# Kernel optimization log

Measured on AMD Instinct MI355X. Metric: run time of the kernel, lower is better.

## Reference

```python
import jax, jax.numpy as jnp
import numpy as np

B, T, C = 1, 4096, 1024
H = 16
D = C // H  # 64
LN_EPS = 1e-5


def layer_norm(x, g, b):
    mu = jnp.mean(x, axis=-1, keepdims=True)
    var = jnp.mean(jnp.square(x - mu), axis=-1, keepdims=True)
    return (x - mu) * jax.lax.rsqrt(var + LN_EPS) * g + b


def setup_inputs() -> dict:
    key = jax.random.key(0)
    ks = jax.random.split(key, 8)
    s = 0.02
    return {
        "x": jax.random.normal(ks[0], (B, T, C), dtype=jnp.float32),
        "ln1_g": jnp.ones((C,), jnp.float32),
        "ln1_b": jnp.zeros((C,), jnp.float32),
        "Wqkv": jax.random.normal(ks[1], (C, 3 * C), dtype=jnp.float32) * s,
        "bqkv": jnp.zeros((3 * C,), jnp.float32),
        "Wo": jax.random.normal(ks[2], (C, C), dtype=jnp.float32) * s,
        "bo": jnp.zeros((C,), jnp.float32),
        "ln2_g": jnp.ones((C,), jnp.float32),
        "ln2_b": jnp.zeros((C,), jnp.float32),
        "W1": jax.random.normal(ks[3], (C, 4 * C), dtype=jnp.float32) * s,
        "b1": jnp.zeros((4 * C,), jnp.float32),
        "W2": jax.random.normal(ks[4], (4 * C, C), dtype=jnp.float32) * s,
        "b2": jnp.zeros((C,), jnp.float32),
    }


def reference(x, ln1_g, ln1_b, Wqkv, bqkv, Wo, bo, ln2_g, ln2_b, W1, b1, W2, b2):
    b, t, c = x.shape
    x_norm = layer_norm(x, ln1_g, ln1_b)
    qkv = x_norm @ Wqkv + bqkv                      # [B,T,3C]
    qkv = qkv.reshape(b, t, 3, H, D).transpose(2, 0, 3, 1, 4)  # [3,B,H,T,D]
    Q, K, V = qkv[0], qkv[1], qkv[2]
    scores = jnp.einsum("bhtd,bhsd->bhts", Q, K) / jnp.sqrt(jnp.float32(D))
    causal = jnp.tril(jnp.ones((t, t), dtype=bool))  # [T,T]
    scores = jnp.where(causal[None, None], scores, -jnp.inf)
    weights = jax.nn.softmax(scores, axis=-1)
    attn = jnp.einsum("bhts,bhsd->bhtd", weights, V)  # [B,H,T,D]
    attn = attn.transpose(0, 2, 1, 3).reshape(b, t, c)
    x = x + (attn @ Wo + bo)
    h = layer_norm(x, ln2_g, ln2_b)
    h = jax.nn.gelu(h @ W1 + b1, approximate=False) @ W2 + b2
    return x + h
```

## Files before the change

### kernel.cpp

```cpp
#include <hip/hip_runtime.h>
#include <math.h>

typedef __bf16 bf16_t;
typedef __attribute__((ext_vector_type(8))) __bf16 bf16x8;
typedef __attribute__((ext_vector_type(4))) __bf16 bf16x4;
typedef __attribute__((ext_vector_type(4))) float f32x4;
typedef __attribute__((ext_vector_type(16))) float f32x16;
typedef __attribute__((ext_vector_type(4))) unsigned int u32x4;

#define T_LEN 4096
#define C_DIM 1024
#define NH 16
#define HD 64

__device__ __forceinline__ void gload_lds16(const void* g, void* l) {
    __builtin_amdgcn_global_load_lds(
        (__attribute__((address_space(1))) void*)(g),
        (__attribute__((address_space(3))) void*)(l), 16, 0, 0);
}

__device__ __forceinline__ f32x4 mfma16(bf16x8 a, bf16x8 b, f32x4 c) {
    return __builtin_amdgcn_mfma_f32_16x16x32_bf16(a, b, c, 0, 0, 0);
}

__device__ __forceinline__ f32x16 mfma32(bf16x8 a, bf16x8 b, f32x16 c) {
    return __builtin_amdgcn_mfma_f32_32x32x16_bf16(a, b, c, 0, 0, 0);
}

__device__ __forceinline__ float gelu_exact(float v) {
    return 0.5f * v * (1.0f + erff(v * 0.7071067811865476f));
}

__device__ __forceinline__ void make_frags2(const f32x16 s, bf16x8& fx, bf16x8& fy) {
    unsigned a0, a1, b0, b1;
    asm("v_cvt_pk_bf16_f32 %0, %1, %2" : "=v"(a0) : "v"(s[0]), "v"(s[1]));
    asm("v_cvt_pk_bf16_f32 %0, %1, %2" : "=v"(a1) : "v"(s[2]), "v"(s[3]));
    asm("v_cvt_pk_bf16_f32 %0, %1, %2" : "=v"(b0) : "v"(s[4]), "v"(s[5]));
    asm("v_cvt_pk_bf16_f32 %0, %1, %2" : "=v"(b1) : "v"(s[6]), "v"(s[7]));
    asm("v_permlane32_swap_b32 %0, %1" : "+v"(a0), "+v"(b0));
    asm("v_permlane32_swap_b32 %0, %1" : "+v"(a1), "+v"(b1));
    u32x4 wa = {a0, a1, b0, b1};
    fx = __builtin_bit_cast(bf16x8, wa);
    unsigned c0, c1, d0, d1;
    asm("v_cvt_pk_bf16_f32 %0, %1, %2" : "=v"(c0) : "v"(s[8]), "v"(s[9]));
    asm("v_cvt_pk_bf16_f32 %0, %1, %2" : "=v"(c1) : "v"(s[10]), "v"(s[11]));
    asm("v_cvt_pk_bf16_f32 %0, %1, %2" : "=v"(d0) : "v"(s[12]), "v"(s[13]));
    asm("v_cvt_pk_bf16_f32 %0, %1, %2" : "=v"(d1) : "v"(s[14]), "v"(s[15]));
    asm("v_permlane32_swap_b32 %0, %1" : "+v"(c0), "+v"(d0));
    asm("v_permlane32_swap_b32 %0, %1" : "+v"(c1), "+v"(d1));
    u32x4 wb = {c0, c1, d0, d1};
    fy = __builtin_bit_cast(bf16x8, wb);
}

__global__ __launch_bounds__(256) void transpose_all(
    const float* __restrict__ wqkv, const float* __restrict__ wo,
    const float* __restrict__ w1, const float* __restrict__ w2,
    bf16_t* __restrict__ oqkv, bf16_t* __restrict__ owo,
    bf16_t* __restrict__ ow1, bf16_t* __restrict__ ow2)
{
    __shared__ float tile[32][33];
    int s = blockIdx.x;
    const float* in; bf16_t* out; int R, C, NBX;
    if (s < 3072)      {            in = wqkv; out = oqkv; R = 1024; C = 3072; NBX = 96; }
    else if (s < 4096) { s -= 3072; in = wo;   out = owo;  R = 1024; C = 1024; NBX = 32; }
    else if (s < 8192) { s -= 4096; in = w1;   out = ow1;  R = 1024; C = 4096; NBX = 128; }
    else               { s -= 8192; in = w2;   out = ow2;  R = 4096; C = 1024; NBX = 32; }
    const int tx = threadIdx.x, ty = threadIdx.y;
    const int c0 = (s % NBX) * 32, r0 = (s / NBX) * 32;
#pragma unroll
    for (int j = 0; j < 4; ++j)
        tile[ty + j * 8][tx] = in[(size_t)(r0 + ty + j * 8) * C + c0 + tx];
    __syncthreads();
#pragma unroll
    for (int j = 0; j < 4; ++j)
        out[(size_t)(c0 + ty + j * 8) * R + r0 + tx] = (bf16_t)tile[tx][ty + j * 8];
}

__global__ __launch_bounds__(256) void vtrans(
    const bf16_t* __restrict__ qkv, bf16_t* __restrict__ vt)
{
    __shared__ bf16_t tile[32][33];
    const int tx = threadIdx.x, ty = threadIdx.y;
    const int h = blockIdx.z;
    const int t0 = blockIdx.x * 32, d0 = blockIdx.y * 32;
#pragma unroll
    for (int j = 0; j < 4; ++j)
        tile[ty + j * 8][tx] =
            qkv[(size_t)(t0 + ty + j * 8) * 3072 + 2048 + h * 64 + d0 + tx];
    __syncthreads();
#pragma unroll
    for (int j = 0; j < 4; ++j)
        vt[(size_t)h * (64 * 4096) + (size_t)(d0 + ty + j * 8) * 4096 + t0 + tx] =
            tile[tx][ty + j * 8];
}

__global__ __launch_bounds__(256) void ln_bf16(
    const float* __restrict__ x, const float* __restrict__ gam,
    const float* __restrict__ bet, bf16_t* __restrict__ out)
{
    const int row = blockIdx.x, t = threadIdx.x;
    const float4 v = *(const float4*)(x + (size_t)row * 1024 + t * 4);
    float s1 = v.x + v.y + v.z + v.w;
    float s2 = v.x * v.x + v.y * v.y + v.z * v.z + v.w * v.w;
#pragma unroll
    for (int m = 1; m < 64; m <<= 1) {
        s1 += __shfl_xor(s1, m);
        s2 += __shfl_xor(s2, m);
    }
    __shared__ float red[8];
    if ((t & 63) == 0) { red[(t >> 6) * 2] = s1; red[(t >> 6) * 2 + 1] = s2; }
    __syncthreads();
    s1 = red[0] + red[2] + red[4] + red[6];
    s2 = red[1] + red[3] + red[5] + red[7];
    const float mu = s1 * (1.0f / 1024.0f);
    const float inv = rsqrtf(s2 * (1.0f / 1024.0f) - mu * mu + 1e-5f);
    const float4 gg = *(const float4*)(gam + t * 4);
    const float4 bb = *(const float4*)(bet + t * 4);
    bf16x4 o;
    o[0] = (bf16_t)((v.x - mu) * inv * gg.x + bb.x);
    o[1] = (bf16_t)((v.y - mu) * inv * gg.y + bb.y);
    o[2] = (bf16_t)((v.z - mu) * inv * gg.z + bb.z);
    o[3] = (bf16_t)((v.w - mu) * inv * gg.w + bb.w);
    *(bf16x4*)(out + (size_t)row * 1024 + t * 4) = o;
}

template <int EPI>
__global__ __launch_bounds__(256, 2) void gemm_bt(
    const bf16_t* __restrict__ A, const bf16_t* __restrict__ Bt,
    const float* __restrict__ bias, const float* __restrict__ res,
    bf16_t* __restrict__ outb, float* __restrict__ outf,
    int M, int N, int Klen, int Kstr)
{
    __shared__ alignas(1024) bf16_t Alds[4][128 * 32];
    __shared__ alignas(1024) bf16_t Blds[4][128 * 32];
    const int t = threadIdx.x;
    const int lane = t & 63, w = t >> 6;
    const int wr = w >> 1, wc = w & 1;
    const int g = lane >> 4, ci = lane & 15;

    int bx, by, chunk = 0;
    if constexpr (EPI == 3) {
        const int flat = blockIdx.x + 8 * blockIdx.y;
        const int xcd = flat & 7, s = flat >> 3;
        chunk = s >> 5;
        const int s2 = s & 31;
        by = xcd * 4 + (s2 >> 3);
        bx = s2 & 7;
        A  += (size_t)chunk * Klen;
        Bt += (size_t)chunk * Klen;
    } else {
        const int NB = gridDim.x, MB = gridDim.y;
        const int flat = blockIdx.x + NB * blockIdx.y;
        const int xcd = flat & 7, slot = flat >> 3;
        by = xcd * (MB >> 3) + slot / NB;
        bx = slot % NB;
    }
    const int m0 = by * 128, n0 = bx * 128;

    f32x4 acc[4][4];
#pragma unroll
    for (int i = 0; i < 4; ++i)
#pragma unroll
        for (int j = 0; j < 4; ++j)
#pragma unroll
            for (int k = 0; k < 4; ++k) acc[i][j][k] = 0.0f;

    const int r0 = t >> 2;
    const int cc = (t & 3) * 8;
    const int nkt = Klen >> 5;

    auto stage = [&](int kt) {
        const int b = kt & 3;
        const int kk = kt * 32;
        char* aB = (char*)&Alds[b][0] + w * 1024;
        char* bB = (char*)&Blds[b][0] + w * 1024;
        gload_lds16(A + (size_t)(m0 + r0) * Kstr + kk + cc, aB);
        gload_lds16(A + (size_t)(m0 + r0 + 64) * Kstr + kk + cc, aB + 4096);
        gload_lds16(Bt + (size_t)(n0 + r0) * Kstr + kk + cc, bB);
        gload_lds16(Bt + (size_t)(n0 + r0 + 64) * Kstr + kk + cc, bB + 4096);
    };

    stage(0);
    if (nkt > 1) stage(1);
    for (int kt = 0; kt < nkt; ++kt) {
        if (kt + 2 < nkt) {
            stage(kt + 2);
            asm volatile("s_waitcnt vmcnt(8)" ::: "memory");
        } else if (kt + 1 < nkt) {
            asm volatile("s_waitcnt vmcnt(4)" ::: "memory");
        } else {
            asm volatile("s_waitcnt vmcnt(0)" ::: "memory");
        }
        __builtin_amdgcn_s_barrier();
        __builtin_amdgcn_sched_barrier(0);
        const int b = kt & 3;
        const bf16_t* ap = &Alds[b][0] + (wr * 64 + ci) * 32 + g * 8;
        const bf16_t* bp = &Blds[b][0] + (wc * 64 + ci) * 32 + g * 8;
        bf16x8 af[4], bf[4];
#pragma unroll
        for (int mt = 0; mt < 4; ++mt) af[mt] = *(const bf16x8*)(ap + mt * 16 * 32);
#pragma unroll
        for (int nt = 0; nt < 4; ++nt) bf[nt] = *(const bf16x8*)(bp + nt * 16 * 32);
        __builtin_amdgcn_s_setprio(1);
#pragma unroll
        for (int mt = 0; mt < 4; ++mt)
#pragma unroll
            for (int nt = 0; nt < 4; ++nt)
                acc[mt][nt] = mfma16(af[mt], bf[nt], acc[mt][nt]);
        __builtin_amdgcn_s_setprio(0);
    }

#pragma unroll
    for (int nt = 0; nt < 4; ++nt) {
        const int col = n0 + wc * 64 + nt * 16 + ci;
        const float bv = (EPI == 3) ? 0.0f : bias[col];
#pragma unroll
        for (int mt = 0; mt < 4; ++mt) {
            const int row = m0 + wr * 64 + mt * 16 + g * 4;
#pragma unroll
            for (int r = 0; r < 4; ++r) {
                float v = acc[mt][nt][r] + bv;
                if constexpr (EPI == 1) v = gelu_exact(v);
                if constexpr (EPI == 2) {
                    outf[(size_t)(row + r) * N + col] =
                        v + res[(size_t)(row + r) * N + col];
                } else if constexpr (EPI == 3) {
                    outf[((size_t)chunk * M + row + r) * N + col] = v;
                } else {
                    outb[(size_t)(row + r) * N + col] = (bf16_t)v;
                }
            }
        }
    }
}

__global__ __launch_bounds__(256) void w2_combine(
    const float* __restrict__ part, const float* __restrict__ bias,
    const float* __restrict__ res, float* __restrict__ out)
{
    const int row = blockIdx.x, t = threadIdx.x;
    const int c = t * 4;
    const float4 a = *(const float4*)(part + (size_t)row * 1024 + c);
    const float4 b = *(const float4*)(part + ((size_t)T_LEN + row) * 1024 + c);
    const float4 rr = *(const float4*)(res + (size_t)row * 1024 + c);
    const float4 bb = *(const float4*)(bias + c);
    float4 o;
    o.x = a.x + b.x + rr.x + bb.x;
    o.y = a.y + b.y + rr.y + bb.y;
    o.z = a.z + b.z + rr.z + bb.z;
    o.w = a.w + b.w + rr.w + bb.w;
    *(float4*)(out + (size_t)row * 1024 + c) = o;
}

template <int EPI>
__global__ __launch_bounds__(512, 2) void gemm256(
    const bf16_t* __restrict__ A, const bf16_t* __restrict__ Bt,
    const float* __restrict__ bias, bf16_t* __restrict__ outb,
    int M, int N, int K)
{
    __shared__ alignas(1024) bf16_t lds[2][2][256 * 64];
    const int t = threadIdx.x, lane = t & 63, w = t >> 6;
    const int g = lane >> 4, ci = lane & 15;
    const int wr = w >> 2, wc = w & 3;
    const int NB = gridDim.x;
    const int nwg = NB * gridDim.y;
    const int flat = blockIdx.x + NB * blockIdx.y;
    const int rix = (flat & 7) * (nwg >> 3) + (flat >> 3);
    const int m0 = (rix / NB) * 256, n0 = (rix % NB) * 256;
    const int NKT = K >> 6;

    f32x4 acc[8][4];
#pragma unroll
    for (int i = 0; i < 8; ++i)
#pragma unroll
        for (int j = 0; j < 4; ++j)
#pragma unroll
            for (int k2 = 0; k2 < 4; ++k2) acc[i][j][k2] = 0.0f;

    const int sw0 = (g ^ (ci & 7)) * 8;
    const int sw1 = ((4 + g) ^ (ci & 7)) * 8;

    auto stage = [&](int h, int ktile, int b) {
#pragma unroll
        for (int i = 0; i < 2; ++i) {
            const int idx = i * 512 + t;
            const int r = idx >> 3;
            const int c = (t & 7) ^ (r & 7);
            const bf16_t* src = ((h < 2) ? A : Bt)
                + (size_t)(((h < 2) ? m0 : n0) + (h & 1) * 128 + r) * K
                + ktile * 64 + c * 8;
            bf16_t* dst = &lds[b][h >> 1][(h & 1) * 8192] + (i * 512 + w * 64) * 8;
            gload_lds16(src, dst);
        }
    };

    bf16x8 a[4][2], b2[2][2][2];

    stage(0, 0, 0); stage(3, 0, 0); stage(1, 0, 0); stage(2, 0, 0);
    if (NKT > 1) { stage(0, 1, 1); stage(3, 1, 1); stage(1, 1, 1); }
    asm volatile("s_waitcnt vmcnt(6)" ::: "memory");
    __builtin_amdgcn_s_barrier();

    for (int kt = 0; kt < NKT; ++kt) {
        const int cur = kt & 1;
        const bf16_t* Ab = &lds[cur][0][0];
        const bf16_t* Bb = &lds[cur][1][0];

#pragma unroll
        for (int mi = 0; mi < 4; ++mi) {
            const bf16_t* ap = Ab + (wr * 64 + mi * 16 + ci) * 64;
            a[mi][0] = *(const bf16x8*)(ap + sw0);
            a[mi][1] = *(const bf16x8*)(ap + sw1);
        }
#pragma unroll
        for (int ni = 0; ni < 2; ++ni) {
            const bf16_t* bp = Bb + (wc * 32 + ni * 16 + ci) * 64;
            b2[0][ni][0] = *(const bf16x8*)(bp + sw0);
            b2[0][ni][1] = *(const bf16x8*)(bp + sw1);
        }
        if (kt + 1 < NKT) stage(2, kt + 1, cur ^ 1);
        __builtin_amdgcn_s_barrier();
        asm volatile("s_waitcnt lgkmcnt(0)" ::: "memory");
        __builtin_amdgcn_sched_barrier(0);
        __builtin_amdgcn_s_setprio(1);
#pragma unroll
        for (int mi = 0; mi < 4; ++mi)
#pragma unroll
            for (int ni = 0; ni < 2; ++ni) {
                acc[mi][ni] = mfma16(a[mi][0], b2[0][ni][0], acc[mi][ni]);
                acc[mi][ni] = mfma16(a[mi][1], b2[0][ni][1], acc[mi][ni]);
            }
        __builtin_amdgcn_s_setprio(0);
        __builtin_amdgcn_s_barrier();

#pragma unroll
        for (int ni = 0; ni < 2; ++ni) {
            const bf16_t* bp = Bb + (128 + wc * 32 + ni * 16 + ci) * 64;
            b2[1][ni][0] = *(const bf16x8*)(bp + sw0);
            b2[1][ni][1] = *(const bf16x8*)(bp + sw1);
        }
        if (kt + 2 < NKT) stage(0, kt + 2, cur);
        __builtin_amdgcn_s_barrier();
        asm volatile("s_waitcnt lgkmcnt(0)" ::: "memory");
        __builtin_amdgcn_sched_barrier(0);
        __builtin_amdgcn_s_setprio(1);
#pragma unroll
        for (int mi = 0; mi < 4; ++mi)
#pragma unroll
            for (int ni = 0; ni < 2; ++ni) {
                acc[mi][2 + ni] = mfma16(a[mi][0], b2[1][ni][0], acc[mi][2 + ni]);
                acc[mi][2 + ni] = mfma16(a[mi][1], b2[1][ni][1], acc[mi][2 + ni]);
            }
        __builtin_amdgcn_s_setprio(0);
        __builtin_amdgcn_s_barrier();

#pragma unroll
        for (int mi = 0; mi < 4; ++mi) {
            const bf16_t* ap = Ab + (128 + wr * 64 + mi * 16 + ci) * 64;
            a[mi][0] = *(const bf16x8*)(ap + sw0);
            a[mi][1] = *(const bf16x8*)(ap + sw1);
        }
        if (kt + 2 < NKT) stage(3, kt + 2, cur);
        __builtin_amdgcn_s_barrier();
        asm volatile("s_waitcnt lgkmcnt(0)" ::: "memory");
        __builtin_amdgcn_sched_barrier(0);
        __builtin_amdgcn_s_setprio(1);
#pragma unroll
        for (int mi = 0; mi < 4; ++mi)
#pragma unroll
            for (int ni = 0; ni < 2; ++ni) {
                acc[4 + mi][2 + ni] = mfma16(a[mi][0], b2[1][ni][0], acc[4 + mi][2 + ni]);
                acc[4 + mi][2 + ni] = mfma16(a[mi][1], b2[1][ni][1], acc[4 + mi][2 + ni]);
            }
        __builtin_amdgcn_s_setprio(0);
        __builtin_amdgcn_s_barrier();

        if (kt + 2 < NKT) stage(1, kt + 2, cur);
        __builtin_amdgcn_s_barrier();
        __builtin_amdgcn_s_setprio(1);
#pragma unroll
        for (int mi = 0; mi < 4; ++mi)
#pragma unroll
            for (int ni = 0; ni < 2; ++ni) {
                acc[4 + mi][ni] = mfma16(a[mi][0], b2[0][ni][0], acc[4 + mi][ni]);
                acc[4 + mi][ni] = mfma16(a[mi][1], b2[0][ni][1], acc[4 + mi][ni]);
            }
        __builtin_amdgcn_s_setprio(0);
        if (kt + 2 < NKT) asm volatile("s_waitcnt vmcnt(6)" ::: "memory");
        else              asm volatile("s_waitcnt vmcnt(0)" ::: "memory");
        __builtin_amdgcn_s_barrier();
    }

#pragma unroll
    for (int mrep = 0; mrep < 8; ++mrep) {
        const int row = m0 + (mrep >> 2) * 128 + wr * 64 + (mrep & 3) * 16 + g * 4;
#pragma unroll
        for (int nrep = 0; nrep < 4; ++nrep) {
            const int col = n0 + (nrep >> 1) * 128 + wc * 32 + (nrep & 1) * 16 + ci;
            const float bv = bias[col];
#pragma unroll
            for (int jr = 0; jr < 4; ++jr) {
                float v = acc[mrep][nrep][jr] + bv;
                if constexpr (EPI == 1) v = gelu_exact(v);
                outb[(size_t)(row + jr) * N + col] = (bf16_t)v;
            }
        }
    }
}

__global__ __launch_bounds__(256, 2) void attn_fwd(
    const bf16_t* __restrict__ qkv, const bf16_t* __restrict__ vt,
    bf16_t* __restrict__ opart, float* __restrict__ mlbuf)
{
    __shared__ alignas(1024) bf16_t Klds[2][64 * 64];
    __shared__ alignas(1024) bf16_t Vlds[2][64 * 64];
    const int t = threadIdx.x, lane = t & 63, w = t >> 6;
    const int hi = lane >> 5, li = lane & 31;
    const int lq = li >> 2;
    const int h = blockIdx.x;
    const int y = blockIdx.y;
    const int jj = y >> 4, v = y & 15;
    const int chunk = jj >> 1;
    const int qt = (jj == 0) ? v : (jj == 1) ? (31 - v) : (jj == 2) ? (16 + v) : (15 - v);
    const int q0 = qt * 128;
    const int qrow = q0 + w * 32 + li;
    const int wDiag = 2 * qt + (w >> 1);
    const int ktA = chunk ? (qt + 1) : 0;
    const int ktB = chunk ? (2 * qt + 2) : (qt + 1);
    const float C1 = 0.125f * 1.4426950408889634f;
    const float FM = 16.0f;

    bf16x8 qf[4];
#pragma unroll
    for (int ks = 0; ks < 4; ++ks)
        qf[ks] = *(const bf16x8*)(qkv + (size_t)qrow * 3072 + h * 64 + ks * 16 + hi * 8);
    bf16x8 ones8;
#pragma unroll
    for (int j = 0; j < 8; ++j) ones8[j] = (bf16_t)1.0f;

    f32x16 oacc[2], lacc;
#pragma unroll
    for (int r = 0; r < 16; ++r) { oacc[0][r] = 0.0f; oacc[1][r] = 0.0f; lacc[r] = 0.0f; }

    const int sr = t >> 3;
    const int sx = ((t & 7) ^ ((sr >> 2) & 7)) * 8;

    auto stageKV = [&](int kt, int b) {
        const size_t kbase = (size_t)(kt * 64) * 3072 + 1024 + h * 64 + sx;
        const size_t vbase = (size_t)h * 262144 + (size_t)kt * 64 + sx;
#pragma unroll
        for (int i = 0; i < 2; ++i) {
            gload_lds16(qkv + kbase + (size_t)(i * 32 + sr) * 3072,
                        (char*)&Klds[b][0] + (size_t)(i * 2048 + t * 8) * 2);
            gload_lds16(vt + vbase + (size_t)(i * 32 + sr) * 4096,
                        (char*)&Vlds[b][0] + (size_t)(i * 2048 + t * 8) * 2);
        }
    };

    stageKV(ktA, 0);
    for (int kt = ktA; kt < ktB; ++kt) {
        const int cur = (kt - ktA) & 1;
        asm volatile("s_waitcnt vmcnt(0)" ::: "memory");
        __syncthreads();
        if (kt + 1 < ktB) stageKV(kt + 1, cur ^ 1);

        if (kt <= wDiag) {
            const bf16_t* Kb = &Klds[cur][0];
            const bf16_t* Vb = &Vlds[cur][0];
            f32x16 s0, s1;
#pragma unroll
            for (int r = 0; r < 16; ++r) { s0[r] = 0.0f; s1[r] = 0.0f; }

            __builtin_amdgcn_s_setprio(1);
#pragma unroll
            for (int ks = 0; ks < 4; ++ks) {
                const int cs = ((ks * 2 + hi) ^ lq) * 8;
                s0 = mfma32(*(const bf16x8*)(Kb + li * 64 + cs), qf[ks], s0);
                s1 = mfma32(*(const bf16x8*)(Kb + (32 + li) * 64 + cs), qf[ks], s1);
            }
            __builtin_amdgcn_s_setprio(0);

            bf16x8 vf[4][2];
#pragma unroll
            for (int ks = 0; ks < 4; ++ks) {
                const int cs = ((ks * 2 + hi) ^ lq) * 8;
                vf[ks][0] = *(const bf16x8*)(Vb + li * 64 + cs);
                vf[ks][1] = *(const bf16x8*)(Vb + (32 + li) * 64 + cs);
            }

            if (kt == wDiag) {
                const int kb0 = kt * 64 + 4 * hi;
#pragma unroll
                for (int r = 0; r < 16; ++r) {
                    const int kp0 = kb0 + (r & 3) + 8 * (r >> 2);
                    if (kp0 > qrow) s0[r] = -1e30f;
                    if (kp0 + 32 > qrow) s1[r] = -1e30f;
                }
            }
#pragma unroll
            for (int r = 0; r < 16; ++r) {
                s0[r] = exp2f(fmaf(s0[r], C1, -FM));
                s1[r] = exp2f(fmaf(s1[r], C1, -FM));
            }

            bf16x8 pf[4];
            make_frags2(s0, pf[0], pf[1]);
            make_frags2(s1, pf[2], pf[3]);

            __builtin_amdgcn_s_setprio(1);
#pragma unroll
            for (int ks = 0; ks < 4; ++ks) {
                oacc[0] = mfma32(vf[ks][0], pf[ks], oacc[0]);
                oacc[1] = mfma32(vf[ks][1], pf[ks], oacc[1]);
                lacc    = mfma32(ones8,     pf[ks], lacc);
            }
            __builtin_amdgcn_s_setprio(0);
        }
        __syncthreads();
    }

    bf16_t* op = opart + ((size_t)chunk * T_LEN + qrow) * 1024 + h * 64 + hi * 4;
#pragma unroll
    for (int dblk = 0; dblk < 2; ++dblk)
#pragma unroll
        for (int gi = 0; gi < 4; ++gi) {
            bf16x4 o4;
#pragma unroll
            for (int j = 0; j < 4; ++j) o4[j] = (bf16_t)oacc[dblk][gi * 4 + j];
            *(bf16x4*)(op + dblk * 32 + gi * 8) = o4;
        }
    if (hi == 0) {
        float2 ml = make_float2(FM, lacc[0]);
        *(float2*)(mlbuf + (((size_t)chunk * T_LEN + qrow) * NH + h) * 2) = ml;
    }
}

__global__ __launch_bounds__(256) void attn_combine(
    const bf16_t* __restrict__ opart, const float* __restrict__ mlbuf,
    bf16_t* __restrict__ out)
{
    const int row = blockIdx.x, t = threadIdx.x;
    const int c = t * 4, h = c >> 6;
    const float2 ml0 = *(const float2*)(mlbuf + ((size_t)row * NH + h) * 2);
    const float2 ml1 = *(const float2*)(mlbuf + (((size_t)T_LEN + row) * NH + h) * 2);
    const float M = fmaxf(ml0.x, ml1.x);
    const float w0 = exp2f(ml0.x - M), w1 = exp2f(ml1.x - M);
    const float inv = 1.0f / (ml0.y * w0 + ml1.y * w1);
    const bf16x4 o0 = *(const bf16x4*)(opart + (size_t)row * 1024 + c);
    const bf16x4 o1 = *(const bf16x4*)(opart + ((size_t)T_LEN + row) * 1024 + c);
    bf16x4 o;
#pragma unroll
    for (int j = 0; j < 4; ++j)
        o[j] = (bf16_t)(((float)o0[j] * w0 + (float)o1[j] * w1) * inv);
    *(bf16x4*)(out + (size_t)row * 1024 + c) = o;
}

extern "C" void kernel_launch(void* const* d_in, const int* in_sizes, int n_in,
                              void* d_out, int out_size, void* d_ws, size_t ws_size,
                              hipStream_t stream)
{
    const float* x    = (const float*)d_in[0];
    const float* ln1g = (const float*)d_in[1];
    const float* ln1b = (const float*)d_in[2];
    const float* Wqkv = (const float*)d_in[3];
    const float* bqkv = (const float*)d_in[4];
    const float* Wo   = (const float*)d_in[5];
    const float* bo   = (const float*)d_in[6];
    const float* ln2g = (const float*)d_in[7];
    const float* ln2b = (const float*)d_in[8];
    const float* W1   = (const float*)d_in[9];
    const float* b1   = (const float*)d_in[10];
    const float* W2   = (const float*)d_in[11];
    const float* b2   = (const float*)d_in[12];
    float* outp = (float*)d_out;

    char* p = (char*)d_ws;
    bf16_t* WqkvT = (bf16_t*)p; p += (size_t)3072 * 1024 * 2;
    bf16_t* WoT   = (bf16_t*)p; p += (size_t)1024 * 1024 * 2;
    bf16_t* W1T   = (bf16_t*)p; p += (size_t)4096 * 1024 * 2;
    bf16_t* W2T   = (bf16_t*)p; p += (size_t)1024 * 4096 * 2;
    bf16_t* xn    = (bf16_t*)p; p += (size_t)4096 * 1024 * 2;
    bf16_t* qkv   = (bf16_t*)p; p += (size_t)4096 * 3072 * 2;
    bf16_t* vtb   = (bf16_t*)p; p += (size_t)16 * 64 * 4096 * 2;
    bf16_t* attnb = (bf16_t*)p; p += (size_t)4096 * 1024 * 2;
    float*  x2    = (float*)p;  p += (size_t)4096 * 1024 * 4;
    bf16_t* hb    = (bf16_t*)p; p += (size_t)4096 * 1024 * 2;
    bf16_t* g1    = (bf16_t*)p; p += (size_t)4096 * 4096 * 2;
    bf16_t* opart = (bf16_t*)p; p += (size_t)2 * 4096 * 1024 * 2;
    float*  mlbuf = (float*)p;  p += (size_t)2 * 4096 * 16 * 2 * 4;
    float*  w2part = (float*)p; p += (size_t)2 * 4096 * 1024 * 4;

    transpose_all<<<12288, dim3(32, 8), 0, stream>>>(Wqkv, Wo, W1, W2,
                                                     WqkvT, WoT, W1T, W2T);

    ln_bf16<<<4096, 256, 0, stream>>>(x, ln1g, ln1b, xn);
    gemm256<0><<<dim3(12, 16), 512, 0, stream>>>(xn, WqkvT, bqkv,
                                                 qkv, 4096, 3072, 1024);
    vtrans<<<dim3(128, 2, 16), dim3(32, 8), 0, stream>>>(qkv, vtb);
    attn_fwd<<<dim3(16, 64), 256, 0, stream>>>(qkv, vtb, opart, mlbuf);
    attn_combine<<<4096, 256, 0, stream>>>(opart, mlbuf, attnb);
    gemm_bt<2><<<dim3(8, 32), 256, 0, stream>>>(attnb, WoT, bo, x,
                                                nullptr, x2, 4096, 1024, 1024, 1024);
    ln_bf16<<<4096, 256, 0, stream>>>(x2, ln2g, ln2b, hb);
    gemm256<1><<<dim3(16, 16), 512, 0, stream>>>(hb, W1T, b1,
                                                 g1, 4096, 4096, 1024);
    gemm_bt<3><<<dim3(8, 64), 256, 0, stream>>>(g1, W2T, nullptr, nullptr,
                                                nullptr, w2part, 4096, 1024, 2048, 4096);
    w2_combine<<<4096, 256, 0, stream>>>(w2part, b2, x2, outp);
}
```

Measured before the change: 271.5 us.

## Fuse V transpose into QKV GEMM epilogue and simplify attention split combine

The QKV GEMM epilogue now writes the V columns straight into the per-head transposed layout, so the separate vtrans kernel and its extra read/write of V go away. Attention drops the stored running max because it uses a fixed max constant (FM), so the combine just adds the two partial outputs and the two row sums. The attention grid now visits query tiles from the heaviest first, with the two chunks interleaved, instead of the old balanced permutation. Risks: the V stores in the epilogue are scattered 8-byte writes, and the fixed-max softmax relies on scores staying within range.

Result: faster. 256.9 us (-5.4%).

```diff
diff --git a/kernel.cpp b/kernel.cpp
--- a/kernel.cpp
+++ b/kernel.cpp
@@ -76,24 +76,6 @@
         out[(size_t)(c0 + ty + j * 8) * R + r0 + tx] = (bf16_t)tile[tx][ty + j * 8];
 }
 
-__global__ __launch_bounds__(256) void vtrans(
-    const bf16_t* __restrict__ qkv, bf16_t* __restrict__ vt)
-{
-    __shared__ bf16_t tile[32][33];
-    const int tx = threadIdx.x, ty = threadIdx.y;
-    const int h = blockIdx.z;
-    const int t0 = blockIdx.x * 32, d0 = blockIdx.y * 32;
-#pragma unroll
-    for (int j = 0; j < 4; ++j)
-        tile[ty + j * 8][tx] =
-            qkv[(size_t)(t0 + ty + j * 8) * 3072 + 2048 + h * 64 + d0 + tx];
-    __syncthreads();
-#pragma unroll
-    for (int j = 0; j < 4; ++j)
-        vt[(size_t)h * (64 * 4096) + (size_t)(d0 + ty + j * 8) * 4096 + t0 + tx] =
-            tile[tx][ty + j * 8];
-}
-
 __global__ __launch_bounds__(256) void ln_bf16(
     const float* __restrict__ x, const float* __restrict__ gam,
     const float* __restrict__ bet, bf16_t* __restrict__ out)
@@ -256,7 +238,7 @@
 __global__ __launch_bounds__(512, 2) void gemm256(
     const bf16_t* __restrict__ A, const bf16_t* __restrict__ Bt,
     const float* __restrict__ bias, bf16_t* __restrict__ outb,
-    int M, int N, int K)
+    bf16_t* __restrict__ vtout, int M, int N, int K)
 {
     __shared__ alignas(1024) bf16_t lds[2][2][256 * 64];
     const int t = threadIdx.x, lane = t & 63, w = t >> 6;
@@ -398,11 +380,21 @@
         for (int nrep = 0; nrep < 4; ++nrep) {
             const int col = n0 + (nrep >> 1) * 128 + wc * 32 + (nrep & 1) * 16 + ci;
             const float bv = bias[col];
-#pragma unroll
-            for (int jr = 0; jr < 4; ++jr) {
-                float v = acc[mrep][nrep][jr] + bv;
-                if constexpr (EPI == 1) v = gelu_exact(v);
-                outb[(size_t)(row + jr) * N + col] = (bf16_t)v;
+            if (EPI == 2 && col >= 2048) {
+                const int cv = col - 2048;
+                bf16x4 o4;
+#pragma unroll
+                for (int jr = 0; jr < 4; ++jr)
+                    o4[jr] = (bf16_t)(acc[mrep][nrep][jr] + bv);
+                *(bf16x4*)(vtout + (size_t)(cv >> 6) * 262144
+                           + (size_t)(cv & 63) * 4096 + row) = o4;
+            } else {
+#pragma unroll
+                for (int jr = 0; jr < 4; ++jr) {
+                    float v = acc[mrep][nrep][jr] + bv;
+                    if constexpr (EPI == 1) v = gelu_exact(v);
+                    outb[(size_t)(row + jr) * N + col] = (bf16_t)v;
+                }
             }
         }
     }
@@ -410,7 +402,7 @@
 
 __global__ __launch_bounds__(256, 2) void attn_fwd(
     const bf16_t* __restrict__ qkv, const bf16_t* __restrict__ vt,
-    bf16_t* __restrict__ opart, float* __restrict__ mlbuf)
+    bf16_t* __restrict__ opart, float* __restrict__ lbuf)
 {
     __shared__ alignas(1024) bf16_t Klds[2][64 * 64];
     __shared__ alignas(1024) bf16_t Vlds[2][64 * 64];
@@ -419,9 +411,8 @@
     const int lq = li >> 2;
     const int h = blockIdx.x;
     const int y = blockIdx.y;
-    const int jj = y >> 4, v = y & 15;
-    const int chunk = jj >> 1;
-    const int qt = (jj == 0) ? v : (jj == 1) ? (31 - v) : (jj == 2) ? (16 + v) : (15 - v);
+    const int qt = 31 - (y >> 1);
+    const int chunk = y & 1;
     const int q0 = qt * 128;
     const int qrow = q0 + w * 32 + li;
     const int wDiag = 2 * qt + (w >> 1);
@@ -529,29 +520,25 @@
             for (int j = 0; j < 4; ++j) o4[j] = (bf16_t)oacc[dblk][gi * 4 + j];
             *(bf16x4*)(op + dblk * 32 + gi * 8) = o4;
         }
-    if (hi == 0) {
-        float2 ml = make_float2(FM, lacc[0]);
-        *(float2*)(mlbuf + (((size_t)chunk * T_LEN + qrow) * NH + h) * 2) = ml;
-    }
+    if (hi == 0)
+        lbuf[((size_t)chunk * T_LEN + qrow) * NH + h] = lacc[0];
 }
 
 __global__ __launch_bounds__(256) void attn_combine(
-    const bf16_t* __restrict__ opart, const float* __restrict__ mlbuf,
+    const bf16_t* __restrict__ opart, const float* __restrict__ lbuf,
     bf16_t* __restrict__ out)
 {
     const int row = blockIdx.x, t = threadIdx.x;
     const int c = t * 4, h = c >> 6;
-    const float2 ml0 = *(const float2*)(mlbuf + ((size_t)row * NH + h) * 2);
-    const float2 ml1 = *(const float2*)(mlbuf + (((size_t)T_LEN + row) * NH + h) * 2);
-    const float M = fmaxf(ml0.x, ml1.x);
-    const float w0 = exp2f(ml0.x - M), w1 = exp2f(ml1.x - M);
-    const float inv = 1.0f / (ml0.y * w0 + ml1.y * w1);
+    const float l0 = lbuf[(size_t)row * NH + h];
+    const float l1 = lbuf[((size_t)T_LEN + row) * NH + h];
+    const float inv = 1.0f / (l0 + l1);
     const bf16x4 o0 = *(const bf16x4*)(opart + (size_t)row * 1024 + c);
     const bf16x4 o1 = *(const bf16x4*)(opart + ((size_t)T_LEN + row) * 1024 + c);
     bf16x4 o;
 #pragma unroll
     for (int j = 0; j < 4; ++j)
-        o[j] = (bf16_t)(((float)o0[j] * w0 + (float)o1[j] * w1) * inv);
+        o[j] = (bf16_t)(((float)o0[j] + (float)o1[j]) * inv);
     *(bf16x4*)(out + (size_t)row * 1024 + c) = o;
 }
 
@@ -587,23 +574,22 @@
     bf16_t* hb    = (bf16_t*)p; p += (size_t)4096 * 1024 * 2;
     bf16_t* g1    = (bf16_t*)p; p += (size_t)4096 * 4096 * 2;
     bf16_t* opart = (bf16_t*)p; p += (size_t)2 * 4096 * 1024 * 2;
-    float*  mlbuf = (float*)p;  p += (size_t)2 * 4096 * 16 * 2 * 4;
+    float*  lbuf  = (float*)p;  p += (size_t)2 * 4096 * 16 * 4;
     float*  w2part = (float*)p; p += (size_t)2 * 4096 * 1024 * 4;
 
     transpose_all<<<12288, dim3(32, 8), 0, stream>>>(Wqkv, Wo, W1, W2,
                                                      WqkvT, WoT, W1T, W2T);
 
     ln_bf16<<<4096, 256, 0, stream>>>(x, ln1g, ln1b, xn);
-    gemm256<0><<<dim3(12, 16), 512, 0, stream>>>(xn, WqkvT, bqkv,
-                                                 qkv, 4096, 3072, 1024);
-    vtrans<<<dim3(128, 2, 16), dim3(32, 8), 0, stream>>>(qkv, vtb);
-    attn_fwd<<<dim3(16, 64), 256, 0, stream>>>(qkv, vtb, opart, mlbuf);
-    attn_combine<<<4096, 256, 0, stream>>>(opart, mlbuf, attnb);
+    gemm256<2><<<dim3(12, 16), 512, 0, stream>>>(xn, WqkvT, bqkv,
+                                                 qkv, vtb, 4096, 3072, 1024);
+    attn_fwd<<<dim3(16, 64), 256, 0, stream>>>(qkv, vtb, opart, lbuf);
+    attn_combine<<<4096, 256, 0, stream>>>(opart, lbuf, attnb);
     gemm_bt<2><<<dim3(8, 32), 256, 0, stream>>>(attnb, WoT, bo, x,
                                                 nullptr, x2, 4096, 1024, 1024, 1024);
     ln_bf16<<<4096, 256, 0, stream>>>(x2, ln2g, ln2b, hb);
     gemm256<1><<<dim3(16, 16), 512, 0, stream>>>(hb, W1T, b1,
-                                                 g1, 4096, 4096, 1024);
+                                                 g1, nullptr, 4096, 4096, 1024);
     gemm_bt<3><<<dim3(8, 64), 256, 0, stream>>>(g1, W2T, nullptr, nullptr,
                                                 nullptr, w2part, 4096, 1024, 2048, 4096);
     w2_combine<<<4096, 256, 0, stream>>>(w2part, b2, x2, outp);
```
